# Kernel tuning notes

Measured on AMD Instinct MI355X. Metric: run time of the kernel, lower is better.

The kernel has to match this reference:

```python
import jax, jax.numpy as jnp
import numpy as np

U = 3  # GRU units

def _gru_scan(x, kernel, rec_kernel, bias):
    # x: [B, S, F]; kernel: [F, 3U]; rec_kernel: [U, 3U]; bias: [2, 3U]
    # Keras GRUCell with reset_after=True (TF2 default).
    B = x.shape[0]
    # Precompute all input projections in one big matmul: [B, S, 3U]
    xk = jnp.einsum('bsf,fg->bsg', x, kernel) + bias[0]
    xk = jnp.transpose(xk, (1, 0, 2))  # [S, B, 3U] for scan over time
    rec_bias = bias[1]

    def step(h, xt):
        inner = h @ rec_kernel + rec_bias                  # [B, 3U]
        xz, xr, xh = jnp.split(xt, 3, axis=-1)
        rz, rr, rh = jnp.split(inner, 3, axis=-1)
        z = jax.nn.sigmoid(xz + rz)
        r = jax.nn.sigmoid(xr + rr)
        hh = jnp.tanh(xh + r * rh)
        h_new = z * h + (1.0 - z) * hh
        return h_new, None

    h0 = jnp.zeros((B, U), dtype=x.dtype)
    h_final, _ = jax.lax.scan(step, h0, xk)
    return h_final  # [B, U]


def setup_inputs() -> dict:
    key = jax.random.key(0)
    ks = jax.random.split(key, 6)
    B, S, F = 4096, 256, 64
    return {
        'inputs': jax.random.normal(ks[0], (B, S, F), dtype=jnp.float32),
        'kernel': jax.random.normal(ks[1], (F, 3 * U), dtype=jnp.float32) * 0.1,
        'rec_kernel': jax.random.normal(ks[2], (U, 3 * U), dtype=jnp.float32) * 0.1,
        'bias': jax.random.normal(ks[3], (2, 3 * U), dtype=jnp.float32) * 0.1,
        'dense_w': jax.random.normal(ks[4], (U, 10), dtype=jnp.float32) * 0.1,
        'dense_b': jnp.zeros((10,), dtype=jnp.float32),
    }


def reference(inputs, kernel, rec_kernel, bias, dense_w, dense_b):
    h = _gru_scan(inputs, kernel, rec_kernel, bias)   # [B, U]; Flatten is a no-op
    logits = h @ dense_w + dense_b                     # [B, 10]
    return jax.nn.softmax(logits, axis=-1)
```

## Files before the change

kernel.cpp:

```cpp
#include <hip/hip_runtime.h>

#define BB 4096
#define SS 256
#define FF 64
#define GG 9

#define NEG_LOG2E -1.4426950408889634f
#define TWO_LOG2E  2.8853900817779268f

typedef float f2 __attribute__((ext_vector_type(2)));

#if __has_builtin(__builtin_amdgcn_exp2f)
__device__ __forceinline__ float fast_exp2(float x) { return __builtin_amdgcn_exp2f(x); }
#else
__device__ __forceinline__ float fast_exp2(float x) { return exp2f(x); }
#endif
#if __has_builtin(__builtin_amdgcn_rcpf)
__device__ __forceinline__ float fast_rcp(float x) { return __builtin_amdgcn_rcpf(x); }
#else
__device__ __forceinline__ float fast_rcp(float x) { return 1.0f / x; }
#endif

template <int CTRL>
__device__ __forceinline__ float dpp_f(float v) {
  return __int_as_float(
      __builtin_amdgcn_mov_dpp(__float_as_int(v), CTRL, 0xF, 0xF, true));
}

__global__ __launch_bounds__(64, 1) void fused_gru_kernel(
    const float* __restrict__ x,
    const float* __restrict__ kernel_w,
    const float* __restrict__ rec_kernel,
    const float* __restrict__ bias,
    const float* __restrict__ dense_w,
    const float* __restrict__ dense_b,
    float* __restrict__ out)
{
  const int lane = threadIdx.x;
  const int fl   = lane & 15;
  const int u    = lane & 3;
  const int uc   = (u < 3) ? u : 2;
  const int c    = blockIdx.x * 4 + (lane >> 4);

  f2 w01[4], w23[4], w45[4], w67[4];
  float w8[4];
#pragma unroll
  for (int e = 0; e < 4; ++e) {
    const float* kw = kernel_w + (fl * 4 + e) * GG;
    w01[e] = (f2){kw[0] * NEG_LOG2E, kw[1] * NEG_LOG2E};
    w23[e] = (f2){kw[2] * NEG_LOG2E, kw[3] * NEG_LOG2E};
    w45[e] = (f2){kw[4] * NEG_LOG2E, kw[5] * NEG_LOG2E};
    w67[e] = (f2){kw[6] * TWO_LOG2E, kw[7] * TWO_LOG2E};
    w8[e]  = kw[8] * TWO_LOG2E;
  }

  const float Q = 0.0625f;
  const f2 b01q = {bias[0] * NEG_LOG2E * Q, bias[1] * NEG_LOG2E * Q};
  const f2 b23q = {bias[2] * NEG_LOG2E * Q, bias[3] * NEG_LOG2E * Q};
  const f2 b45q = {bias[4] * NEG_LOG2E * Q, bias[5] * NEG_LOG2E * Q};
  const f2 b67q = {bias[6] * TWO_LOG2E * Q, bias[7] * TWO_LOG2E * Q};
  const float b8q = bias[8] * TWO_LOG2E * Q;

  float wz[3], wr[3], wh[3];
#pragma unroll
  for (int hh = 0; hh < 3; ++hh) {
    wz[hh] = rec_kernel[hh * GG + uc]     * NEG_LOG2E;
    wr[hh] = rec_kernel[hh * GG + 3 + uc] * NEG_LOG2E;
    wh[hh] = rec_kernel[hh * GG + 6 + uc] * TWO_LOG2E;
  }
  const float rbz = bias[GG + uc]     * NEG_LOG2E;
  const float rbr = bias[GG + 3 + uc] * NEG_LOG2E;
  const float rbh = bias[GG + 6 + uc] * TWO_LOG2E;

  float h0 = 0.0f, h1 = 0.0f, h2 = 0.0f, hprev = 0.0f;

  const float4* pc = reinterpret_cast<const float4*>(x) + (size_t)c * SS * 16 + fl;

  float4 X0, X1, X2, X3, X4, X5, X6, X7;

  auto step = [&](const float4 v) {
    f2 a01 = b01q, a23 = b23q, a45 = b45q, a67 = b67q;
    float a8 = b8q;
    a01 = v.x * w01[0] + a01; a23 = v.x * w23[0] + a23;
    a45 = v.x * w45[0] + a45; a67 = v.x * w67[0] + a67;
    a8 = fmaf(v.x, w8[0], a8);
    a01 = v.y * w01[1] + a01; a23 = v.y * w23[1] + a23;
    a45 = v.y * w45[1] + a45; a67 = v.y * w67[1] + a67;
    a8 = fmaf(v.y, w8[1], a8);
    a01 = v.z * w01[2] + a01; a23 = v.z * w23[2] + a23;
    a45 = v.z * w45[2] + a45; a67 = v.z * w67[2] + a67;
    a8 = fmaf(v.z, w8[2], a8);
    a01 = v.w * w01[3] + a01; a23 = v.w * w23[3] + a23;
    a45 = v.w * w45[3] + a45; a67 = v.w * w67[3] + a67;
    a8 = fmaf(v.w, w8[3], a8);

    float s0 = a01.x, s1 = a01.y, s2 = a23.x, s3 = a23.y, s4 = a45.x,
          s5 = a45.y, s6 = a67.x, s7 = a67.y, s8 = a8;
    s0 += dpp_f<0xB1>(s0); s1 += dpp_f<0xB1>(s1); s2 += dpp_f<0xB1>(s2);
    s3 += dpp_f<0xB1>(s3); s4 += dpp_f<0xB1>(s4); s5 += dpp_f<0xB1>(s5);
    s6 += dpp_f<0xB1>(s6); s7 += dpp_f<0xB1>(s7); s8 += dpp_f<0xB1>(s8);
    s0 += dpp_f<0x4E>(s0); s1 += dpp_f<0x4E>(s1); s2 += dpp_f<0x4E>(s2);
    s3 += dpp_f<0x4E>(s3); s4 += dpp_f<0x4E>(s4); s5 += dpp_f<0x4E>(s5);
    s6 += dpp_f<0x4E>(s6); s7 += dpp_f<0x4E>(s7); s8 += dpp_f<0x4E>(s8);
    s0 += dpp_f<0x124>(s0); s1 += dpp_f<0x124>(s1); s2 += dpp_f<0x124>(s2);
    s3 += dpp_f<0x124>(s3); s4 += dpp_f<0x124>(s4); s5 += dpp_f<0x124>(s5);
    s6 += dpp_f<0x124>(s6); s7 += dpp_f<0x124>(s7); s8 += dpp_f<0x124>(s8);
    s0 += dpp_f<0x128>(s0); s1 += dpp_f<0x128>(s1); s2 += dpp_f<0x128>(s2);
    s3 += dpp_f<0x128>(s3); s4 += dpp_f<0x128>(s4); s5 += dpp_f<0x128>(s5);
    s6 += dpp_f<0x128>(s6); s7 += dpp_f<0x128>(s7); s8 += dpp_f<0x128>(s8);

    const float sz = (u == 0) ? s0 : ((u == 1) ? s1 : s2);
    const float sr = (u == 0) ? s3 : ((u == 1) ? s4 : s5);
    const float sh = (u == 0) ? s6 : ((u == 1) ? s7 : s8);
    const float iz = fmaf(h2, wz[2], fmaf(h1, wz[1], fmaf(h0, wz[0], sz + rbz)));
    const float ir = fmaf(h2, wr[2], fmaf(h1, wr[1], fmaf(h0, wr[0], sr + rbr)));
    const float ih = fmaf(h2, wh[2], fmaf(h1, wh[1], fmaf(h0, wh[0], rbh)));
    const float z = fast_rcp(1.0f + fast_exp2(iz));
    const float r = fast_rcp(1.0f + fast_exp2(ir));
    const float t = fmaf(-2.0f, fast_rcp(1.0f + fast_exp2(fmaf(r, ih, sh))), 1.0f);
    const float hn = fmaf(z, hprev - t, t);
    hprev = hn;
    h0 = dpp_f<0x00>(hn);
    h1 = dpp_f<0x55>(hn);
    h2 = dpp_f<0xAA>(hn);
  };

  auto pf = [&](int sn) -> float4 {
    sn = (sn < SS) ? sn : (SS - 1);
    return pc[(size_t)sn * 16];
  };

  X0 = pf(0); X1 = pf(1); X2 = pf(2); X3 = pf(3);
  X4 = pf(4); X5 = pf(5); X6 = pf(6); X7 = pf(7);

  for (int sg = 0; sg < SS; sg += 8) {
    step(X0); X0 = pf(sg + 8);
    step(X1); X1 = pf(sg + 9);
    step(X2); X2 = pf(sg + 10);
    step(X3); X3 = pf(sg + 11);
    step(X4); X4 = pf(sg + 12);
    step(X5); X5 = pf(sg + 13);
    step(X6); X6 = pf(sg + 14);
    step(X7); X7 = pf(sg + 15);
  }

  if (fl < 4) {
    float lg[10];
#pragma unroll
    for (int j = 0; j < 10; ++j)
      lg[j] = dense_b[j] + h0 * dense_w[j] + h1 * dense_w[10 + j] + h2 * dense_w[20 + j];
    float m = lg[0];
#pragma unroll
    for (int j = 1; j < 10; ++j) m = fmaxf(m, lg[j]);
    float e[10];
    float ssum = 0.0f;
#pragma unroll
    for (int j = 0; j < 10; ++j) {
      e[j] = fast_exp2(1.4426950408889634f * (lg[j] - m));
      ssum += e[j];
    }
    const float inv = fast_rcp(ssum);
#pragma unroll
    for (int j = u; j < 10; j += 4) out[(size_t)c * 10 + j] = e[j] * inv;
  }
}

extern "C" void kernel_launch(void* const* d_in, const int* in_sizes, int n_in,
                              void* d_out, int out_size, void* d_ws, size_t ws_size,
                              hipStream_t stream) {
  const float* x      = (const float*)d_in[0];
  const float* kern   = (const float*)d_in[1];
  const float* rkern  = (const float*)d_in[2];
  const float* bias   = (const float*)d_in[3];
  const float* dw     = (const float*)d_in[4];
  const float* db     = (const float*)d_in[5];
  float* out = (float*)d_out;

  fused_gru_kernel<<<BB / 4, 64, 0, stream>>>(x, kern, rkern, bias, dw, db, out);
}
```

Before: 61.02 us.

## Split each batch row across 32 lanes with float2 loads and selective reduction

Each sequence now gets 32 lanes instead of 16, each lane handling 2 features with float2 loads. Grid size doubles to BB/2 blocks and launch bounds allow 2 blocks per CU. The cross-lane reduction is restructured so the first two DPP stages run on all 9 gate sums, and the later stages run only on the 3 selected per-unit sums, with a ds_swizzle xor-16 as the final step. Folding the recurrent z/r biases into the input bias removes two adds per step. The serial recurrence gets shorter per-step arithmetic and more waves for latency hiding, at the cost of the ds_swizzle latency on the critical path and narrower loads.

After: 87.71 us. 1.44x slower.

```diff
diff --git a/kernel.cpp b/kernel.cpp
--- a/kernel.cpp
+++ b/kernel.cpp
@@ -27,7 +27,12 @@
       __builtin_amdgcn_mov_dpp(__float_as_int(v), CTRL, 0xF, 0xF, true));
 }
 
-__global__ __launch_bounds__(64, 1) void fused_gru_kernel(
+__device__ __forceinline__ float swz_xor16(float v) {
+  return __int_as_float(
+      __builtin_amdgcn_ds_swizzle(__float_as_int(v), (16 << 10) | 0x1F));
+}
+
+__global__ __launch_bounds__(64, 2) void fused_gru_kernel(
     const float* __restrict__ x,
     const float* __restrict__ kernel_w,
     const float* __restrict__ rec_kernel,
@@ -37,16 +42,16 @@
     float* __restrict__ out)
 {
   const int lane = threadIdx.x;
-  const int fl   = lane & 15;
+  const int l32  = lane & 31;
   const int u    = lane & 3;
   const int uc   = (u < 3) ? u : 2;
-  const int c    = blockIdx.x * 4 + (lane >> 4);
+  const int c    = blockIdx.x * 2 + (lane >> 5);
 
-  f2 w01[4], w23[4], w45[4], w67[4];
-  float w8[4];
+  f2 w01[2], w23[2], w45[2], w67[2];
+  float w8[2];
 #pragma unroll
-  for (int e = 0; e < 4; ++e) {
-    const float* kw = kernel_w + (fl * 4 + e) * GG;
+  for (int e = 0; e < 2; ++e) {
+    const float* kw = kernel_w + (l32 * 2 + e) * GG;
     w01[e] = (f2){kw[0] * NEG_LOG2E, kw[1] * NEG_LOG2E};
     w23[e] = (f2){kw[2] * NEG_LOG2E, kw[3] * NEG_LOG2E};
     w45[e] = (f2){kw[4] * NEG_LOG2E, kw[5] * NEG_LOG2E};
@@ -54,10 +59,13 @@
     w8[e]  = kw[8] * TWO_LOG2E;
   }
 
-  const float Q = 0.0625f;
-  const f2 b01q = {bias[0] * NEG_LOG2E * Q, bias[1] * NEG_LOG2E * Q};
-  const f2 b23q = {bias[2] * NEG_LOG2E * Q, bias[3] * NEG_LOG2E * Q};
-  const f2 b45q = {bias[4] * NEG_LOG2E * Q, bias[5] * NEG_LOG2E * Q};
+  const float Q = 0.03125f;
+  const f2 b01q = {(bias[0] + bias[GG + 0]) * NEG_LOG2E * Q,
+                   (bias[1] + bias[GG + 1]) * NEG_LOG2E * Q};
+  const f2 b23q = {(bias[2] + bias[GG + 2]) * NEG_LOG2E * Q,
+                   (bias[3] + bias[GG + 3]) * NEG_LOG2E * Q};
+  const f2 b45q = {(bias[4] + bias[GG + 4]) * NEG_LOG2E * Q,
+                   (bias[5] + bias[GG + 5]) * NEG_LOG2E * Q};
   const f2 b67q = {bias[6] * TWO_LOG2E * Q, bias[7] * TWO_LOG2E * Q};
   const float b8q = bias[8] * TWO_LOG2E * Q;
 
@@ -68,17 +76,15 @@
     wr[hh] = rec_kernel[hh * GG + 3 + uc] * NEG_LOG2E;
     wh[hh] = rec_kernel[hh * GG + 6 + uc] * TWO_LOG2E;
   }
-  const float rbz = bias[GG + uc]     * NEG_LOG2E;
-  const float rbr = bias[GG + 3 + uc] * NEG_LOG2E;
   const float rbh = bias[GG + 6 + uc] * TWO_LOG2E;
 
   float h0 = 0.0f, h1 = 0.0f, h2 = 0.0f, hprev = 0.0f;
 
-  const float4* pc = reinterpret_cast<const float4*>(x) + (size_t)c * SS * 16 + fl;
+  const float2* pc = reinterpret_cast<const float2*>(x) + (size_t)c * SS * 32 + l32;
 
-  float4 X0, X1, X2, X3, X4, X5, X6, X7;
+  float2 X0, X1, X2, X3, X4, X5, X6, X7;
 
-  auto step = [&](const float4 v) {
+  auto step = [&](const float2 v) {
     f2 a01 = b01q, a23 = b23q, a45 = b45q, a67 = b67q;
     float a8 = b8q;
     a01 = v.x * w01[0] + a01; a23 = v.x * w23[0] + a23;
@@ -87,12 +93,6 @@
     a01 = v.y * w01[1] + a01; a23 = v.y * w23[1] + a23;
     a45 = v.y * w45[1] + a45; a67 = v.y * w67[1] + a67;
     a8 = fmaf(v.y, w8[1], a8);
-    a01 = v.z * w01[2] + a01; a23 = v.z * w23[2] + a23;
-    a45 = v.z * w45[2] + a45; a67 = v.z * w67[2] + a67;
-    a8 = fmaf(v.z, w8[2], a8);
-    a01 = v.w * w01[3] + a01; a23 = v.w * w23[3] + a23;
-    a45 = v.w * w45[3] + a45; a67 = v.w * w67[3] + a67;
-    a8 = fmaf(v.w, w8[3], a8);
 
     float s0 = a01.x, s1 = a01.y, s2 = a23.x, s3 = a23.y, s4 = a45.x,
           s5 = a45.y, s6 = a67.x, s7 = a67.y, s8 = a8;
@@ -102,18 +102,17 @@
     s0 += dpp_f<0x4E>(s0); s1 += dpp_f<0x4E>(s1); s2 += dpp_f<0x4E>(s2);
     s3 += dpp_f<0x4E>(s3); s4 += dpp_f<0x4E>(s4); s5 += dpp_f<0x4E>(s5);
     s6 += dpp_f<0x4E>(s6); s7 += dpp_f<0x4E>(s7); s8 += dpp_f<0x4E>(s8);
-    s0 += dpp_f<0x124>(s0); s1 += dpp_f<0x124>(s1); s2 += dpp_f<0x124>(s2);
-    s3 += dpp_f<0x124>(s3); s4 += dpp_f<0x124>(s4); s5 += dpp_f<0x124>(s5);
-    s6 += dpp_f<0x124>(s6); s7 += dpp_f<0x124>(s7); s8 += dpp_f<0x124>(s8);
-    s0 += dpp_f<0x128>(s0); s1 += dpp_f<0x128>(s1); s2 += dpp_f<0x128>(s2);
-    s3 += dpp_f<0x128>(s3); s4 += dpp_f<0x128>(s4); s5 += dpp_f<0x128>(s5);
-    s6 += dpp_f<0x128>(s6); s7 += dpp_f<0x128>(s7); s8 += dpp_f<0x128>(s8);
 
-    const float sz = (u == 0) ? s0 : ((u == 1) ? s1 : s2);
-    const float sr = (u == 0) ? s3 : ((u == 1) ? s4 : s5);
-    const float sh = (u == 0) ? s6 : ((u == 1) ? s7 : s8);
-    const float iz = fmaf(h2, wz[2], fmaf(h1, wz[1], fmaf(h0, wz[0], sz + rbz)));
-    const float ir = fmaf(h2, wr[2], fmaf(h1, wr[1], fmaf(h0, wr[0], sr + rbr)));
+    float az = (u == 0) ? s0 : ((u == 1) ? s1 : s2);
+    float ar = (u == 0) ? s3 : ((u == 1) ? s4 : s5);
+    float sh = (u == 0) ? s6 : ((u == 1) ? s7 : s8);
+
+    az += dpp_f<0x124>(az); ar += dpp_f<0x124>(ar); sh += dpp_f<0x124>(sh);
+    az += dpp_f<0x128>(az); ar += dpp_f<0x128>(ar); sh += dpp_f<0x128>(sh);
+    az += swz_xor16(az); ar += swz_xor16(ar); sh += swz_xor16(sh);
+
+    const float iz = fmaf(h2, wz[2], fmaf(h1, wz[1], fmaf(h0, wz[0], az)));
+    const float ir = fmaf(h2, wr[2], fmaf(h1, wr[1], fmaf(h0, wr[0], ar)));
     const float ih = fmaf(h2, wh[2], fmaf(h1, wh[1], fmaf(h0, wh[0], rbh)));
     const float z = fast_rcp(1.0f + fast_exp2(iz));
     const float r = fast_rcp(1.0f + fast_exp2(ir));
@@ -125,9 +124,9 @@
     h2 = dpp_f<0xAA>(hn);
   };
 
-  auto pf = [&](int sn) -> float4 {
+  auto pf = [&](int sn) -> float2 {
     sn = (sn < SS) ? sn : (SS - 1);
-    return pc[(size_t)sn * 16];
+    return pc[(size_t)sn * 32];
   };
 
   X0 = pf(0); X1 = pf(1); X2 = pf(2); X3 = pf(3);
@@ -144,7 +143,7 @@
     step(X7); X7 = pf(sg + 15);
   }
 
-  if (fl < 4) {
+  if (l32 < 4) {
     float lg[10];
 #pragma unroll
     for (int j = 0; j < 10; ++j)
@@ -176,5 +175,5 @@
   const float* db     = (const float*)d_in[5];
   float* out = (float*)d_out;
 
-  fused_gru_kernel<<<BB / 4, 64, 0, stream>>>(x, kern, rkern, bias, dw, db, out);
+  fused_gru_kernel<<<BB / 2, 64, 0, stream>>>(x, kern, rkern, bias, dw, db, out);
 }
```
